# Kernel optimization log

Hardware: AMD Instinct MI355X
Metric: run time of the kernel (lower is better)

The kernel has to match this reference:

```python
import jax, jax.numpy as jnp
import numpy as np

D = 768        # embed_dim
P = 16         # patch_size
DEPTH = 12
FF = 3072      # dim_feedforward = 4*D
NUM_CLASSES = 100
EPS = 1e-5     # nn.LayerNorm default


def _ln(x, g, b):
    m = jnp.mean(x, axis=-1, keepdims=True)
    v = jnp.mean((x - m) ** 2, axis=-1, keepdims=True)
    return (x - m) / jnp.sqrt(v + EPS) * g + b


def setup_inputs() -> dict:
    key = jax.random.key(0)
    ks = jax.random.split(key, 24)
    f32 = jnp.float32
    inp = {
        'x': jax.random.normal(ks[0], (32, 3, 224, 224), dtype=f32),
        # patch embed conv: [C_in, P, P, D] layout for einsum
        'patch_w': jax.random.normal(ks[1], (3, P, P, D), dtype=f32) * 0.02,
        'patch_b': jnp.zeros((D,), f32),
        'cls_token': jax.random.normal(ks[2], (1, 1, D), dtype=f32) * 0.02,
        'pos_embed': jax.random.normal(ks[3], (1, 197, D), dtype=f32) * 0.02,
        # stacked per-layer params; Linear stored as [in, out]
        'Wq': jax.random.normal(ks[4], (DEPTH, D, D), dtype=f32) * 0.02,
        'bq': jnp.zeros((DEPTH, D), f32),
        'Wk': jax.random.normal(ks[5], (DEPTH, D, D), dtype=f32) * 0.02,
        'bk': jnp.zeros((DEPTH, D), f32),
        'Wv': jax.random.normal(ks[6], (DEPTH, D, D), dtype=f32) * 0.02,
        'bv': jnp.zeros((DEPTH, D), f32),
        'W1': jax.random.normal(ks[7], (DEPTH, D, FF), dtype=f32) * 0.02,
        'b1': jnp.zeros((DEPTH, FF), f32),
        'W2': jax.random.normal(ks[8], (DEPTH, FF, D), dtype=f32) * 0.02,
        'b2': jnp.zeros((DEPTH, D), f32),
        'ln1_g': jnp.ones((DEPTH, D), f32),
        'ln1_b': jnp.zeros((DEPTH, D), f32),
        'ln2_g': jnp.ones((DEPTH, D), f32),
        'ln2_b': jnp.zeros((DEPTH, D), f32),
        'lnf_g': jnp.ones((D,), f32),
        'lnf_b': jnp.zeros((D,), f32),
        'head_w': jax.random.normal(ks[9], (D, NUM_CLASSES), dtype=f32) * 0.02,
        'head_b': jnp.zeros((NUM_CLASSES,), f32),
    }
    return inp


def reference(x, patch_w, patch_b, cls_token, pos_embed,
              Wq, bq, Wk, bk, Wv, bv, W1, b1, W2, b2,
              ln1_g, ln1_b, ln2_g, ln2_b, lnf_g, lnf_b,
              head_w, head_b):
    B = x.shape[0]
    Hp = x.shape[2] // P  # 14
    # patch embed: Conv2d(k=16, s=16) == non-overlapping patch projection
    xp = x.reshape(B, 3, Hp, P, Hp, P)
    tok = jnp.einsum('bchpwq,cpqd->bhwd', xp, patch_w).reshape(B, Hp * Hp, D) + patch_b
    tok = jnp.concatenate([jnp.broadcast_to(cls_token, (B, 1, D)), tok], axis=1)
    tok = tok + pos_embed  # [B, 197, D]
    N = tok.shape[1]
    # gumbel noise for F.gumbel_softmax(tau=1, hard=False), one sample per layer
    gnoise = jax.random.gumbel(jax.random.key(1), (DEPTH, B, N, N), dtype=tok.dtype)
    inv_sqrt_d = 1.0 / jnp.sqrt(jnp.asarray(D, tok.dtype))

    def step(src, p):
        (wq, bq_, wk, bk_, wv, bv_, w1, b1_, w2, b2_,
         g1, be1, g2, be2, gn) = p
        Q = src @ wq + bq_
        K = src @ wk + bk_
        V = src @ wv + bv_
        scores = jnp.einsum('bnd,bmd->bnm', Q, K) * inv_sqrt_d
        attn = jax.nn.softmax(scores + gn, axis=-1) @ V
        src = _ln(src + attn, g1, be1)          # note: out_linear unused in source
        ff = jax.nn.gelu(src @ w1 + b1_, approximate=False) @ w2 + b2_
        src = _ln(src + ff, g2, be2)
        return src, None

    xs = (Wq, bq, Wk, bk, Wv, bv, W1, b1, W2, b2,
          ln1_g, ln1_b, ln2_g, ln2_b, gnoise)
    tok, _ = jax.lax.scan(step, tok, xs)
    tok = _ln(tok, lnf_g, lnf_b)
    cls = tok[:, 0]
    return cls @ head_w + head_b
```

## Files before the change

### kernel.cpp

```cpp
#include <hip/hip_runtime.h>
#include <hip/hip_bf16.h>
#include <math.h>


namespace {
constexpr int DIM    = 768;
constexpr int FF_DIM = 3072;
constexpr int QKVN   = 2304;
constexpr int NTOK   = 197;
constexpr int NBATCH = 32;
constexpr int NLAYER = 12;
constexpr int ROWS   = NBATCH * NTOK;
constexpr int NPATCH = 196;
constexpr int PROWS  = NBATCH * NPATCH;
constexpr int KVPAD  = 256;
constexpr float LN_EPS = 1e-5f;
}

typedef __attribute__((ext_vector_type(8))) __bf16 bf16x8;
typedef __attribute__((ext_vector_type(4))) float  f32x4;

__device__ __forceinline__ unsigned rotl32(unsigned v, int d) {
  return (v << d) | (v >> (32 - d));
}

__device__ __forceinline__ float gumbel_noise(unsigned idx) {
  const unsigned ks0 = 0u, ks1 = 1u, ks2 = 0x1BD11BDBu;
  unsigned x0 = 0u + ks0;
  unsigned x1 = idx + ks1;
#define TFR(r) { x0 += x1; x1 = rotl32(x1, (r)); x1 ^= x0; }
  TFR(13) TFR(15) TFR(26) TFR(6)   x0 += ks1; x1 += ks2 + 1u;
  TFR(17) TFR(29) TFR(16) TFR(24)  x0 += ks2; x1 += ks0 + 2u;
  TFR(13) TFR(15) TFR(26) TFR(6)   x0 += ks0; x1 += ks1 + 3u;
  TFR(17) TFR(29) TFR(16) TFR(24)  x0 += ks1; x1 += ks2 + 4u;
  TFR(13) TFR(15) TFR(26) TFR(6)   x0 += ks2; x1 += ks0 + 5u;
#undef TFR
  unsigned bits = x0 ^ x1;
  float f = __uint_as_float((bits >> 9) | 0x3f800000u) - 1.0f;
  const float tiny = 1.17549435e-38f;
  float u = fmaxf(tiny, f + tiny);
  return -logf(-logf(u));
}

__device__ __forceinline__ float block_reduce_sum(float val, float* red) {
  int tid = threadIdx.x;
  red[tid] = val; __syncthreads();
  for (int off = 128; off > 0; off >>= 1) {
    if (tid < off) red[tid] += red[tid + off];
    __syncthreads();
  }
  float r = red[0];
  __syncthreads();
  return r;
}

__device__ __forceinline__ float block_reduce_max(float val, float* red) {
  int tid = threadIdx.x;
  red[tid] = val; __syncthreads();
  for (int off = 128; off > 0; off >>= 1) {
    if (tid < off) red[tid] = fmaxf(red[tid], red[tid + off]);
    __syncthreads();
  }
  float r = red[0];
  __syncthreads();
  return r;
}

__device__ __forceinline__ void async_copy16(const void* g, void* l) {
  __builtin_amdgcn_global_load_lds(
      (const __attribute__((address_space(1))) unsigned*)g,
      (__attribute__((address_space(3))) unsigned*)l, 16, 0, 0);
}

__device__ __forceinline__ int xcd_swizzle(int id, int nwg) {
  const int q = nwg >> 3, r = nwg & 7;
  const int xcd = id & 7, pos = id >> 3;
  return (xcd < r ? xcd * (q + 1) : r * (q + 1) + (xcd - r) * q) + pos;
}

template<int STORE, bool GELU>
__global__ void mm_nt(
    const __hip_bfloat16* __restrict__ A, long sA, int lda,
    const __hip_bfloat16* __restrict__ B, long sB, int ldb,
    void* __restrict__ Cv, long sC, int ldc,
    int M, int N, int K, const float* __restrict__ bias) {
  __shared__ __hip_bfloat16 As[128 * 64];
  __shared__ __hip_bfloat16 Bs[128 * 64];
  const int bz = blockIdx.y;
  A += (long)bz * sA;
  B += (long)bz * sB;
  const int tilesN = (N + 127) >> 7;
  const int id = xcd_swizzle(blockIdx.x, gridDim.x);
  const int row0 = (id / tilesN) * 128, col0 = (id % tilesN) * 128;

  const int tid = threadIdx.x, lane = tid & 63, wid = tid >> 6;
  const int wr = (wid >> 1) * 64, wc = (wid & 1) * 64;
  const int fr = lane & 15;
  const int kh = lane >> 4;
  const int fsw = fr & 7;
  f32x4 acc[4][4] = {};

  const int elem = wid * 512 + lane * 8;

  for (int k0 = 0; k0 < K; k0 += 64) {
    #pragma unroll
    for (int c = 0; c < 4; c++) {
      const int e = c * 2048 + elem;
      const int r = e >> 6;
      const int slot = (e >> 3) & 7;
      const int ksw = ((slot ^ (r & 7)) << 3);
      async_copy16(A + (long)(row0 + r) * lda + k0 + ksw,
                   (char*)As + c * 4096 + wid * 1024);
    }
    #pragma unroll
    for (int c = 0; c < 4; c++) {
      const int e = c * 2048 + elem;
      const int r = e >> 6;
      const int slot = (e >> 3) & 7;
      const int ksw = ((slot ^ (r & 7)) << 3);
      async_copy16(B + (long)(col0 + r) * ldb + k0 + ksw,
                   (char*)Bs + c * 4096 + wid * 1024);
    }
    __syncthreads();
    #pragma unroll
    for (int ks = 0; ks < 2; ks++) {
      bf16x8 a[4], b[4];
      #pragma unroll
      for (int i = 0; i < 4; i++) {
        const int row = wr + i * 16 + fr;
        const int sl  = ((ks << 2) | kh) ^ fsw;
        a[i] = *(const bf16x8*)((const char*)As + row * 128 + (sl << 4));
      }
      #pragma unroll
      for (int j = 0; j < 4; j++) {
        const int row = wc + j * 16 + fr;
        const int sl  = ((ks << 2) | kh) ^ fsw;
        b[j] = *(const bf16x8*)((const char*)Bs + row * 128 + (sl << 4));
      }
      #pragma unroll
      for (int i = 0; i < 4; i++)
        #pragma unroll
        for (int j = 0; j < 4; j++)
          acc[i][j] = __builtin_amdgcn_mfma_f32_16x16x32_bf16(
              a[i], b[j], acc[i][j], 0, 0, 0);
    }
    __syncthreads();
  }

  #pragma unroll
  for (int i = 0; i < 4; i++) {
    #pragma unroll
    for (int j = 0; j < 4; j++) {
      #pragma unroll
      for (int t = 0; t < 4; t++) {
        const int r  = row0 + wr + i * 16 + kh * 4 + t;
        const int cc = col0 + wc + j * 16 + fr;
        if (r < M && cc < N) {
          float v = acc[i][j][t];
          if (bias) v += bias[cc];
          if (GELU) v = 0.5f * v * (1.0f + erff(v * 0.70710678118654752f));
          if (STORE == 0)
            ((float*)Cv)[(long)bz * sC + (long)r * ldc + cc] = v;
          else
            ((__hip_bfloat16*)Cv)[(long)bz * sC + (long)r * ldc + cc] =
                __float2bfloat16(v);
        }
      }
    }
  }
}

__global__ void transpose_bf16_kernel(const float* __restrict__ W,
                                      __hip_bfloat16* __restrict__ Wt,
                                      int K, int N) {
  __shared__ float t[32][33];
  const int k0 = blockIdx.x * 32, n0 = blockIdx.y * 32;
  const int tx = threadIdx.x & 31, ty = threadIdx.x >> 5;
  #pragma unroll
  for (int i = 0; i < 32; i += 8)
    t[ty + i][tx] = W[(long)(k0 + ty + i) * N + n0 + tx];
  __syncthreads();
  #pragma unroll
  for (int i = 0; i < 32; i += 8)
    Wt[(long)(n0 + ty + i) * K + k0 + tx] = __float2bfloat16(t[tx][ty + i]);
}

__global__ void wtrans_layer(const float* __restrict__ Wq,
                             const float* __restrict__ Wk,
                             const float* __restrict__ Wv,
                             const float* __restrict__ W1,
                             const float* __restrict__ W2,
                             __hip_bfloat16* __restrict__ wqkv_t,
                             __hip_bfloat16* __restrict__ w1_t,
                             __hip_bfloat16* __restrict__ w2_t) {
  __shared__ float t[32][33];
  const int id = blockIdx.x;
  const float* W; __hip_bfloat16* O; int K, N, k0, n0;
  if (id < 1728) {
    const int m = id / 576, tt = id % 576;
    W = (m == 0) ? Wq : (m == 1) ? Wk : Wv;
    O = wqkv_t + (long)m * DIM * DIM;
    K = DIM; N = DIM; k0 = (tt / 24) * 32; n0 = (tt % 24) * 32;
  } else if (id < 4032) {
    const int tt = id - 1728;
    W = W1; O = w1_t;
    K = DIM; N = FF_DIM; k0 = (tt / 96) * 32; n0 = (tt % 96) * 32;
  } else {
    const int tt = id - 4032;
    W = W2; O = w2_t;
    K = FF_DIM; N = DIM; k0 = (tt / 24) * 32; n0 = (tt % 24) * 32;
  }
  const int tx = threadIdx.x & 31, ty = threadIdx.x >> 5;
  #pragma unroll
  for (int i = 0; i < 32; i += 8)
    t[ty + i][tx] = W[(long)(k0 + ty + i) * N + n0 + tx];
  __syncthreads();
  #pragma unroll
  for (int i = 0; i < 32; i += 8)
    O[(long)(n0 + ty + i) * K + k0 + tx] = __float2bfloat16(t[tx][ty + i]);
}

__global__ void build_qkv_bias(const float* __restrict__ bq,
                               const float* __restrict__ bk,
                               const float* __restrict__ bv,
                               float* __restrict__ o) {
  const int l = blockIdx.x;
  for (int d = threadIdx.x; d < DIM; d += 256) {
    o[l * QKVN + d]           = bq[l * DIM + d];
    o[l * QKVN + DIM + d]     = bk[l * DIM + d];
    o[l * QKVN + 2 * DIM + d] = bv[l * DIM + d];
  }
}

__global__ void vtrans_kernel(const __hip_bfloat16* __restrict__ qkv,
                              __hip_bfloat16* __restrict__ vt) {
  __shared__ __hip_bfloat16 s[64][68];
  const int b = blockIdx.z;
  const int t0 = blockIdx.x * 64;
  const int d0 = blockIdx.y * 64;
  const int tx = threadIdx.x & 63, ty = threadIdx.x >> 6;
  for (int i = ty; i < 64; i += 4) {
    const int t = t0 + i;
    __hip_bfloat16 v = __float2bfloat16(0.f);
    if (t < NTOK) v = qkv[(long)(b * NTOK + t) * QKVN + 2 * DIM + d0 + tx];
    s[i][tx] = v;
  }
  __syncthreads();
  for (int i = ty; i < 64; i += 4)
    vt[((long)b * DIM + d0 + i) * KVPAD + t0 + tx] = s[tx][i];
}

__global__ void im2col_kernel(const float* __restrict__ x,
                              __hip_bfloat16* __restrict__ col) {
  const int p = blockIdx.x;
  const int b = p / NPATCH, pi = p % NPATCH;
  const int h = pi / 14, w = pi % 14;
  for (int e = threadIdx.x; e < DIM; e += 256) {
    const int c = e >> 8, r = e & 255, pp = r >> 4, q = r & 15;
    col[(long)p * DIM + e] = __float2bfloat16(
        x[(((long)b * 3 + c) * 224 + h * 16 + pp) * 224 + w * 16 + q]);
  }
}

__global__ void assemble_kernel(const float* __restrict__ tmp,
                                const float* __restrict__ cls,
                                const float* __restrict__ pos,
                                float* __restrict__ tok,
                                __hip_bfloat16* __restrict__ tok_bf) {
  const int row = blockIdx.x;
  const int b = row / NTOK, n = row % NTOK;
  for (int d = threadIdx.x; d < DIM; d += 256) {
    float v = (n == 0) ? cls[d] : tmp[(long)(b * NPATCH + n - 1) * DIM + d];
    v += pos[n * DIM + d];
    tok[(long)row * DIM + d] = v;
    tok_bf[(long)row * DIM + d] = __float2bfloat16(v);
  }
}

__global__ void softmax_kernel(const float* __restrict__ sc,
                               __hip_bfloat16* __restrict__ P, int layer) {
  __shared__ float red[256];
  const int row = blockIdx.x;
  const int b = row / NTOK, n = row % NTOK;
  const int tid = threadIdx.x;
  const long base = (long)row * NTOK;
  const float inv_sqrt_d = 0.036084391824351615f;

  float x = -INFINITY;
  if (tid < NTOK) {
    const unsigned idx =
        ((((unsigned)layer * NBATCH + b) * NTOK + n) * NTOK) + tid;
    x = sc[base + tid] * inv_sqrt_d + gumbel_noise(idx);
  }
  const float mx = block_reduce_max(x, red);
  float ex = (tid < NTOK) ? expf(x - mx) : 0.f;
  const float s = block_reduce_sum(ex, red);
  const float pv = (tid < NTOK) ? ex / s : 0.f;
  P[(long)row * KVPAD + tid] = __float2bfloat16(pv);
}

__global__ void add_ln_kernel(float* __restrict__ tok,
                              __hip_bfloat16* __restrict__ tok_bf,
                              const float* __restrict__ res,
                              const float* __restrict__ g,
                              const float* __restrict__ beta) {
  __shared__ float red[256];
  const int row = blockIdx.x;
  const int tid = threadIdx.x;
  const long base = (long)row * DIM;
  float v[3];
  float s = 0.f;
  #pragma unroll
  for (int i = 0; i < 3; i++) {
    const int d = tid + (i << 8);
    v[i] = tok[base + d] + res[base + d];
    s += v[i];
  }
  const float mean = block_reduce_sum(s, red) * (1.0f / DIM);
  float s2 = 0.f;
  #pragma unroll
  for (int i = 0; i < 3; i++) { const float dd = v[i] - mean; s2 += dd * dd; }
  const float var = block_reduce_sum(s2, red) * (1.0f / DIM);
  const float inv = 1.0f / sqrtf(var + LN_EPS);
  #pragma unroll
  for (int i = 0; i < 3; i++) {
    const int d = tid + (i << 8);
    const float o = (v[i] - mean) * inv * g[d] + beta[d];
    tok[base + d] = o;
    tok_bf[base + d] = __float2bfloat16(o);
  }
}

__global__ void head_kernel(const float* __restrict__ tok,
                            const float* __restrict__ g,
                            const float* __restrict__ beta,
                            const float* __restrict__ hw,
                            const float* __restrict__ hb,
                            float* __restrict__ out) {
  __shared__ float red[256];
  __shared__ float xn[DIM];
  const int b = blockIdx.x;
  const int tid = threadIdx.x;
  const float* xr = tok + (long)b * NTOK * DIM;
  float v[3];
  float s = 0.f;
  #pragma unroll
  for (int i = 0; i < 3; i++) { v[i] = xr[tid + (i << 8)]; s += v[i]; }
  const float mean = block_reduce_sum(s, red) * (1.0f / DIM);
  float s2 = 0.f;
  #pragma unroll
  for (int i = 0; i < 3; i++) { const float dd = v[i] - mean; s2 += dd * dd; }
  const float var = block_reduce_sum(s2, red) * (1.0f / DIM);
  const float inv = 1.0f / sqrtf(var + LN_EPS);
  #pragma unroll
  for (int i = 0; i < 3; i++) {
    const int d = tid + (i << 8);
    xn[d] = (v[i] - mean) * inv * g[d] + beta[d];
  }
  __syncthreads();
  for (int c = tid; c < 100; c += 256) {
    float acc = hb[c];
    for (int d = 0; d < DIM; d++) acc += xn[d] * hw[d * 100 + c];
    out[b * 100 + c] = acc;
  }
}

extern "C" void kernel_launch(void* const* d_in, const int* in_sizes, int n_in,
                              void* d_out, int out_size, void* d_ws, size_t ws_size,
                              hipStream_t stream) {
  const float* x        = (const float*)d_in[0];
  const float* patch_w  = (const float*)d_in[1];
  const float* patch_b  = (const float*)d_in[2];
  const float* cls_tok  = (const float*)d_in[3];
  const float* pos_emb  = (const float*)d_in[4];
  const float* Wq       = (const float*)d_in[5];
  const float* bq       = (const float*)d_in[6];
  const float* Wk       = (const float*)d_in[7];
  const float* bk       = (const float*)d_in[8];
  const float* Wv       = (const float*)d_in[9];
  const float* bv       = (const float*)d_in[10];
  const float* W1       = (const float*)d_in[11];
  const float* b1       = (const float*)d_in[12];
  const float* W2       = (const float*)d_in[13];
  const float* b2       = (const float*)d_in[14];
  const float* ln1_g    = (const float*)d_in[15];
  const float* ln1_b    = (const float*)d_in[16];
  const float* ln2_g    = (const float*)d_in[17];
  const float* ln2_b    = (const float*)d_in[18];
  const float* lnf_g    = (const float*)d_in[19];
  const float* lnf_b    = (const float*)d_in[20];
  const float* head_w   = (const float*)d_in[21];
  const float* head_b   = (const float*)d_in[22];
  float* out = (float*)d_out;

  float* fb = (float*)d_ws;
  long fo = 0;
  float* tok      = fb + fo; fo += 6400L * DIM;
  float* b4       = fb + fo; fo += 6400L * DIM;
  float* scbuf    = fb + fo; fo += 1241920L;
  float* bias_all = fb + fo; fo += (long)NLAYER * QKVN;
  __hip_bfloat16* hbuf = (__hip_bfloat16*)(fb + fo);
  long ho = 0;
  __hip_bfloat16* tok_bf = hbuf + ho; ho += 6400L * DIM;
  __hip_bfloat16* qkv    = hbuf + ho;
  __hip_bfloat16* ffout  = hbuf + ho; ho += 6400L * FF_DIM;
  __hip_bfloat16* vt     = hbuf + ho; ho += (long)NBATCH * DIM * KVPAD;
  __hip_bfloat16* Pb     = hbuf + ho; ho += 6400L * KVPAD;
  __hip_bfloat16* wqkv_t = hbuf + ho; ho += (long)QKVN * DIM;
  __hip_bfloat16* w1_t   = hbuf + ho; ho += (long)FF_DIM * DIM;
  __hip_bfloat16* w2_t   = hbuf + ho; ho += (long)DIM * FF_DIM;

  const long DD = (long)DIM * DIM;
  const long QKVSTRIDE = (long)NTOK * QKVN;
  const long TOKSTRIDE = (long)NTOK * DIM;
  const long SCSTRIDE  = (long)NTOK * NTOK;
  const long VTSTRIDE  = (long)DIM * KVPAD;
  const long PSTRIDE   = (long)NTOK * KVPAD;

  build_qkv_bias<<<NLAYER, 256, 0, stream>>>(bq, bk, bv, bias_all);

  im2col_kernel<<<PROWS, 256, 0, stream>>>(x, ffout);
  transpose_bf16_kernel<<<dim3(DIM / 32, DIM / 32), 256, 0, stream>>>(
      patch_w, wqkv_t, DIM, DIM);
  mm_nt<0, false><<<dim3(49 * 6, 1), 256, 0, stream>>>(
      ffout, 0, DIM, wqkv_t, 0, DIM, b4, 0, DIM, PROWS, DIM, DIM, patch_b);
  assemble_kernel<<<ROWS, 256, 0, stream>>>(b4, cls_tok, pos_emb, tok, tok_bf);

  for (int l = 0; l < NLAYER; l++) {
    wtrans_layer<<<6336, 256, 0, stream>>>(
        Wq + l * DD, Wk + l * DD, Wv + l * DD,
        W1 + (long)l * DIM * FF_DIM, W2 + (long)l * FF_DIM * DIM,
        wqkv_t, w1_t, w2_t);

    mm_nt<1, false><<<dim3(50 * (QKVN / 128), 1), 256, 0, stream>>>(
        tok_bf, 0, DIM, wqkv_t, 0, DIM, qkv, 0, QKVN,
        ROWS, QKVN, DIM, bias_all + l * QKVN);

    vtrans_kernel<<<dim3(KVPAD / 64, DIM / 64, NBATCH), 256, 0, stream>>>(qkv, vt);

    mm_nt<0, false><<<dim3(2 * 2, NBATCH), 256, 0, stream>>>(
        qkv, QKVSTRIDE, QKVN, qkv + DIM, QKVSTRIDE, QKVN, scbuf, SCSTRIDE, NTOK,
        NTOK, NTOK, DIM, nullptr);

    softmax_kernel<<<ROWS, 256, 0, stream>>>(scbuf, Pb, l);

    mm_nt<0, false><<<dim3(2 * (DIM / 128), NBATCH), 256, 0, stream>>>(
        Pb, PSTRIDE, KVPAD, vt, VTSTRIDE, KVPAD, b4, TOKSTRIDE, DIM,
        NTOK, DIM, KVPAD, nullptr);

    add_ln_kernel<<<ROWS, 256, 0, stream>>>(tok, tok_bf, b4,
        ln1_g + l * DIM, ln1_b + l * DIM);

    mm_nt<1, true><<<dim3(50 * (FF_DIM / 128), 1), 256, 0, stream>>>(
        tok_bf, 0, DIM, w1_t, 0, DIM, ffout, 0, FF_DIM,
        ROWS, FF_DIM, DIM, b1 + l * FF_DIM);
    mm_nt<0, false><<<dim3(50 * (DIM / 128), 1), 256, 0, stream>>>(
        ffout, 0, FF_DIM, w2_t, 0, FF_DIM, b4, 0, DIM,
        ROWS, DIM, FF_DIM, b2 + l * DIM);

    add_ln_kernel<<<ROWS, 256, 0, stream>>>(tok, tok_bf, b4,
        ln2_g + l * DIM, ln2_b + l * DIM);
  }

  head_kernel<<<NBATCH, 256, 0, stream>>>(tok, lnf_g, lnf_b, head_w, head_b, out);
}
```

Before: 3.003 ms.

## Fuse QK^T with gumbel softmax, hoist weight transposes, split-K the FFN down-projection

Replaces the separate scores GEMM and softmax kernels with one attn_sm kernel. It computes QK^T with MFMA and applies scaling, gumbel noise and softmax in registers, so the fp32 score buffer no longer goes through memory. When the workspace is large enough, all layers' weight transposes run in a single launch up front instead of once per layer. The W2 GEMM is split into two K halves that write separate buffers, and their sum plus the bias is folded into the following add+LayerNorm kernel. This raises parallelism at the cost of one extra fp32 activation buffer read and written.

```diff
diff --git a/kernel.cpp b/kernel.cpp
--- a/kernel.cpp
+++ b/kernel.cpp
@@ -47,18 +47,6 @@
   red[tid] = val; __syncthreads();
   for (int off = 128; off > 0; off >>= 1) {
     if (tid < off) red[tid] += red[tid + off];
-    __syncthreads();
-  }
-  float r = red[0];
-  __syncthreads();
-  return r;
-}
-
-__device__ __forceinline__ float block_reduce_max(float val, float* red) {
-  int tid = threadIdx.x;
-  red[tid] = val; __syncthreads();
-  for (int off = 128; off > 0; off >>= 1) {
-    if (tid < off) red[tid] = fmaxf(red[tid], red[tid + off]);
     __syncthreads();
   }
   float r = red[0];
@@ -170,6 +158,89 @@
   }
 }
 
+__global__ __launch_bounds__(256) void attn_sm(
+    const __hip_bfloat16* __restrict__ qkv, long qstride,
+    __hip_bfloat16* __restrict__ Pb, int layer) {
+  __shared__ __hip_bfloat16 As[64 * 64];
+  __shared__ __hip_bfloat16 Bs[256 * 64];
+  const int b = blockIdx.y;
+  const int row0 = blockIdx.x * 64;
+  const __hip_bfloat16* Qb = qkv + (long)b * qstride;
+  const __hip_bfloat16* Kb = Qb + DIM;
+
+  const int tid = threadIdx.x, lane = tid & 63, wid = tid >> 6;
+  const int fr = lane & 15, kh = lane >> 4, fsw = fr & 7;
+  f32x4 acc[16] = {};
+  const int elem = wid * 512 + lane * 8;
+
+  for (int k0 = 0; k0 < DIM; k0 += 64) {
+    #pragma unroll
+    for (int c = 0; c < 2; c++) {
+      const int e = c * 2048 + elem;
+      const int r = e >> 6, slot = (e >> 3) & 7;
+      const int ksw = ((slot ^ (r & 7)) << 3);
+      async_copy16(Qb + (long)(row0 + r) * QKVN + k0 + ksw,
+                   (char*)As + c * 4096 + wid * 1024);
+    }
+    #pragma unroll
+    for (int c = 0; c < 8; c++) {
+      const int e = c * 2048 + elem;
+      const int r = e >> 6, slot = (e >> 3) & 7;
+      const int ksw = ((slot ^ (r & 7)) << 3);
+      async_copy16(Kb + (long)r * QKVN + k0 + ksw,
+                   (char*)Bs + c * 4096 + wid * 1024);
+    }
+    __syncthreads();
+    #pragma unroll
+    for (int ks = 0; ks < 2; ks++) {
+      const int sl = ((ks << 2) | kh) ^ fsw;
+      const bf16x8 a =
+          *(const bf16x8*)((const char*)As + (wid * 16 + fr) * 128 + (sl << 4));
+      #pragma unroll
+      for (int j = 0; j < 16; j++) {
+        const bf16x8 bb =
+            *(const bf16x8*)((const char*)Bs + (j * 16 + fr) * 128 + (sl << 4));
+        acc[j] = __builtin_amdgcn_mfma_f32_16x16x32_bf16(a, bb, acc[j], 0, 0, 0);
+      }
+    }
+    __syncthreads();
+  }
+
+  const float scale = 0.036084391824351615f;
+  #pragma unroll
+  for (int tt = 0; tt < 4; tt++) {
+    const int R = row0 + wid * 16 + kh * 4 + tt;
+    float xs[16];
+    float mx = -INFINITY;
+    #pragma unroll
+    for (int j = 0; j < 16; j++) {
+      const int m = j * 16 + fr;
+      float xx = -INFINITY;
+      if (m < NTOK) {
+        const unsigned idx =
+            (((unsigned)layer * NBATCH + b) * NTOK + (unsigned)R) * NTOK + m;
+        xx = acc[j][tt] * scale + gumbel_noise(idx);
+      }
+      xs[j] = xx;
+      mx = fmaxf(mx, xx);
+    }
+    #pragma unroll
+    for (int o = 1; o < 16; o <<= 1) mx = fmaxf(mx, __shfl_xor(mx, o));
+    float sum = 0.f;
+    #pragma unroll
+    for (int j = 0; j < 16; j++) { xs[j] = expf(xs[j] - mx); sum += xs[j]; }
+    #pragma unroll
+    for (int o = 1; o < 16; o <<= 1) sum += __shfl_xor(sum, o);
+    const float inv = 1.0f / sum;
+    if (R < NTOK) {
+      #pragma unroll
+      for (int j = 0; j < 16; j++)
+        Pb[((long)b * NTOK + R) * KVPAD + j * 16 + fr] =
+            __float2bfloat16(xs[j] * inv);
+    }
+  }
+}
+
 __global__ void transpose_bf16_kernel(const float* __restrict__ W,
                                       __hip_bfloat16* __restrict__ Wt,
                                       int K, int N) {
@@ -185,15 +256,22 @@
     Wt[(long)(n0 + ty + i) * K + k0 + tx] = __float2bfloat16(t[tx][ty + i]);
 }
 
-__global__ void wtrans_layer(const float* __restrict__ Wq,
-                             const float* __restrict__ Wk,
-                             const float* __restrict__ Wv,
-                             const float* __restrict__ W1,
-                             const float* __restrict__ W2,
-                             __hip_bfloat16* __restrict__ wqkv_t,
-                             __hip_bfloat16* __restrict__ w1_t,
-                             __hip_bfloat16* __restrict__ w2_t) {
+__global__ void wtrans_kernel(const float* __restrict__ Wq,
+                              const float* __restrict__ Wk,
+                              const float* __restrict__ Wv,
+                              const float* __restrict__ W1,
+                              const float* __restrict__ W2,
+                              __hip_bfloat16* __restrict__ wqkv_t,
+                              __hip_bfloat16* __restrict__ w1_t,
+                              __hip_bfloat16* __restrict__ w2_t,
+                              long sq, long s1, long s2) {
   __shared__ float t[32][33];
+  const int l = blockIdx.y;
+  Wq += (long)l * DIM * DIM;  Wk += (long)l * DIM * DIM;
+  Wv += (long)l * DIM * DIM;
+  W1 += (long)l * DIM * FF_DIM;  W2 += (long)l * FF_DIM * DIM;
+  wqkv_t += (long)l * sq;  w1_t += (long)l * s1;  w2_t += (long)l * s2;
+
   const int id = blockIdx.x;
   const float* W; __hip_bfloat16* O; int K, N, k0, n0;
   if (id < 1728) {
@@ -277,31 +355,11 @@
   }
 }
 
-__global__ void softmax_kernel(const float* __restrict__ sc,
-                               __hip_bfloat16* __restrict__ P, int layer) {
-  __shared__ float red[256];
-  const int row = blockIdx.x;
-  const int b = row / NTOK, n = row % NTOK;
-  const int tid = threadIdx.x;
-  const long base = (long)row * NTOK;
-  const float inv_sqrt_d = 0.036084391824351615f;
-
-  float x = -INFINITY;
-  if (tid < NTOK) {
-    const unsigned idx =
-        ((((unsigned)layer * NBATCH + b) * NTOK + n) * NTOK) + tid;
-    x = sc[base + tid] * inv_sqrt_d + gumbel_noise(idx);
-  }
-  const float mx = block_reduce_max(x, red);
-  float ex = (tid < NTOK) ? expf(x - mx) : 0.f;
-  const float s = block_reduce_sum(ex, red);
-  const float pv = (tid < NTOK) ? ex / s : 0.f;
-  P[(long)row * KVPAD + tid] = __float2bfloat16(pv);
-}
-
 __global__ void add_ln_kernel(float* __restrict__ tok,
                               __hip_bfloat16* __restrict__ tok_bf,
                               const float* __restrict__ res,
+                              const float* __restrict__ res2,
+                              const float* __restrict__ rbias,
                               const float* __restrict__ g,
                               const float* __restrict__ beta) {
   __shared__ float red[256];
@@ -313,8 +371,11 @@
   #pragma unroll
   for (int i = 0; i < 3; i++) {
     const int d = tid + (i << 8);
-    v[i] = tok[base + d] + res[base + d];
-    s += v[i];
+    float r = tok[base + d] + res[base + d];
+    if (res2)  r += res2[base + d];
+    if (rbias) r += rbias[d];
+    v[i] = r;
+    s += r;
   }
   const float mean = block_reduce_sum(s, red) * (1.0f / DIM);
   float s2 = 0.f;
@@ -393,11 +454,24 @@
   const float* head_b   = (const float*)d_in[22];
   float* out = (float*)d_out;
 
+  const long WQKV = (long)QKVN * DIM;
+  const long W1SZ = (long)FF_DIM * DIM;
+  const long W2SZ = (long)DIM * FF_DIM;
+  const long WLAYER = WQKV + W1SZ + W2SZ;
+
+  const long F32N = 3L * 6400 * DIM + (long)NLAYER * QKVN;
+  const long BF16FIX = 6400L * DIM + 6400L * FF_DIM +
+                       (long)NBATCH * DIM * KVPAD + 6400L * KVPAD +
+                       (long)DIM * DIM;
+  const size_t need12 = (size_t)F32N * 4 + (size_t)(BF16FIX + 12 * WLAYER) * 2;
+  const bool hoist = ws_size >= need12;
+  const int NW = hoist ? NLAYER : 1;
+
   float* fb = (float*)d_ws;
   long fo = 0;
   float* tok      = fb + fo; fo += 6400L * DIM;
   float* b4       = fb + fo; fo += 6400L * DIM;
-  float* scbuf    = fb + fo; fo += 1241920L;
+  float* b4b      = fb + fo; fo += 6400L * DIM;
   float* bias_all = fb + fo; fo += (long)NLAYER * QKVN;
   __hip_bfloat16* hbuf = (__hip_bfloat16*)(fb + fo);
   long ho = 0;
@@ -406,59 +480,66 @@
   __hip_bfloat16* ffout  = hbuf + ho; ho += 6400L * FF_DIM;
   __hip_bfloat16* vt     = hbuf + ho; ho += (long)NBATCH * DIM * KVPAD;
   __hip_bfloat16* Pb     = hbuf + ho; ho += 6400L * KVPAD;
-  __hip_bfloat16* wqkv_t = hbuf + ho; ho += (long)QKVN * DIM;
-  __hip_bfloat16* w1_t   = hbuf + ho; ho += (long)FF_DIM * DIM;
-  __hip_bfloat16* w2_t   = hbuf + ho; ho += (long)DIM * FF_DIM;
+  __hip_bfloat16* pw_t   = hbuf + ho; ho += (long)DIM * DIM;
+  __hip_bfloat16* wqkv_t = hbuf + ho; ho += (long)NW * WQKV;
+  __hip_bfloat16* w1_t   = hbuf + ho; ho += (long)NW * W1SZ;
+  __hip_bfloat16* w2_t   = hbuf + ho; ho += (long)NW * W2SZ;
 
   const long DD = (long)DIM * DIM;
   const long QKVSTRIDE = (long)NTOK * QKVN;
   const long TOKSTRIDE = (long)NTOK * DIM;
-  const long SCSTRIDE  = (long)NTOK * NTOK;
   const long VTSTRIDE  = (long)DIM * KVPAD;
   const long PSTRIDE   = (long)NTOK * KVPAD;
 
   build_qkv_bias<<<NLAYER, 256, 0, stream>>>(bq, bk, bv, bias_all);
 
+  if (hoist) {
+    wtrans_kernel<<<dim3(6336, NLAYER), 256, 0, stream>>>(
+        Wq, Wk, Wv, W1, W2, wqkv_t, w1_t, w2_t, WQKV, W1SZ, W2SZ);
+  }
+
   im2col_kernel<<<PROWS, 256, 0, stream>>>(x, ffout);
   transpose_bf16_kernel<<<dim3(DIM / 32, DIM / 32), 256, 0, stream>>>(
-      patch_w, wqkv_t, DIM, DIM);
+      patch_w, pw_t, DIM, DIM);
   mm_nt<0, false><<<dim3(49 * 6, 1), 256, 0, stream>>>(
-      ffout, 0, DIM, wqkv_t, 0, DIM, b4, 0, DIM, PROWS, DIM, DIM, patch_b);
+      ffout, 0, DIM, pw_t, 0, DIM, b4, 0, DIM, PROWS, DIM, DIM, patch_b);
   assemble_kernel<<<ROWS, 256, 0, stream>>>(b4, cls_tok, pos_emb, tok, tok_bf);
 
   for (int l = 0; l < NLAYER; l++) {
-    wtrans_layer<<<6336, 256, 0, stream>>>(
-        Wq + l * DD, Wk + l * DD, Wv + l * DD,
-        W1 + (long)l * DIM * FF_DIM, W2 + (long)l * FF_DIM * DIM,
-        wqkv_t, w1_t, w2_t);
+    __hip_bfloat16* wqkv_l = wqkv_t + (hoist ? (long)l * WQKV : 0);
+    __hip_bfloat16* w1_l   = w1_t   + (hoist ? (long)l * W1SZ : 0);
+    __hip_bfloat16* w2_l   = w2_t   + (hoist ? (long)l * W2SZ : 0);
+    if (!hoist) {
+      wtrans_kernel<<<dim3(6336, 1), 256, 0, stream>>>(
+          Wq + l * DD, Wk + l * DD, Wv + l * DD,
+          W1 + (long)l * DIM * FF_DIM, W2 + (long)l * FF_DIM * DIM,
+          wqkv_l, w1_l, w2_l, 0, 0, 0);
+    }
 
     mm_nt<1, false><<<dim3(50 * (QKVN / 128), 1), 256, 0, stream>>>(
-        tok_bf, 0, DIM, wqkv_t, 0, DIM, qkv, 0, QKVN,
+        tok_bf, 0, DIM, wqkv_l, 0, DIM, qkv, 0, QKVN,
         ROWS, QKVN, DIM, bias_all + l * QKVN);
 
     vtrans_kernel<<<dim3(KVPAD / 64, DIM / 64, NBATCH), 256, 0, stream>>>(qkv, vt);
 
-    mm_nt<0, false><<<dim3(2 * 2, NBATCH), 256, 0, stream>>>(
-        qkv, QKVSTRIDE, QKVN, qkv + DIM, QKVSTRIDE, QKVN, scbuf, SCSTRIDE, NTOK,
-        NTOK, NTOK, DIM, nullptr);
-
-    softmax_kernel<<<ROWS, 256, 0, stream>>>(scbuf, Pb, l);
+    attn_sm<<<dim3(4, NBATCH), 256, 0, stream>>>(qkv, QKVSTRIDE, Pb, l);
 
     mm_nt<0, false><<<dim3(2 * (DIM / 128), NBATCH), 256, 0, stream>>>(
         Pb, PSTRIDE, KVPAD, vt, VTSTRIDE, KVPAD, b4, TOKSTRIDE, DIM,
         NTOK, DIM, KVPAD, nullptr);
 
-    add_ln_kernel<<<ROWS, 256, 0, stream>>>(tok, tok_bf, b4,
+    add_ln_kernel<<<ROWS, 256, 0, stream>>>(tok, tok_bf, b4, nullptr, nullptr,
         ln1_g + l * DIM, ln1_b + l * DIM);
 
     mm_nt<1, true><<<dim3(50 * (FF_DIM / 128), 1), 256, 0, stream>>>(
-        tok_bf, 0, DIM, w1_t, 0, DIM, ffout, 0, FF_DIM,
+        tok_bf, 0, DIM, w1_l, 0, DIM, ffout, 0, FF_DIM,
         ROWS, FF_DIM, DIM, b1 + l * FF_DIM);
-    mm_nt<0, false><<<dim3(50 * (DIM / 128), 1), 256, 0, stream>>>(
-        ffout, 0, FF_DIM, w2_t, 0, FF_DIM, b4, 0, DIM,
-        ROWS, DIM, FF_DIM, b2 + l * DIM);
-
-    add_ln_kernel<<<ROWS, 256, 0, stream>>>(tok, tok_bf, b4,
+
+    mm_nt<0, false><<<dim3(50 * (DIM / 128), 2), 256, 0, stream>>>(
+        ffout, 1536, FF_DIM, w2_l, 1536, FF_DIM,
+        b4, 6400L * DIM, DIM, ROWS, DIM, 1536, nullptr);
+
+    add_ln_kernel<<<ROWS, 256, 0, stream>>>(tok, tok_bf, b4, b4b, b2 + l * DIM,
         ln2_g + l * DIM, ln2_b + l * DIM);
   }
 
```

Result: slower. 3.654 ms (+21.7%).
